# Optimization experiments

Hardware: AMD Instinct MI355X
Metric: run time of the kernel (lower is better)

Reference implementation:

```python
import jax, jax.numpy as jnp
import numpy as np

B, H, S, D = 4, 16, 2048, 64


def setup_inputs() -> dict:
    key = jax.random.key(0)
    kq, kk, kv = jax.random.split(key, 3)
    Q = jax.random.normal(kq, (B, H, S, D), dtype=jnp.float32)
    K = jax.random.normal(kk, (B, H, S, D), dtype=jnp.float32)
    V = jax.random.normal(kv, (B, H, S, D), dtype=jnp.float32)
    # causal mask, broadcasts over (B, H); True = keep, False (==0) = mask out
    mask = jnp.tril(jnp.ones((S, S), dtype=bool))
    return {"Q": Q, "K": K, "V": V, "mask": mask}


def reference(Q, K, V, mask):
    d_k = Q.shape[-1]
    scale = 1.0 / jnp.sqrt(jnp.asarray(d_k, dtype=Q.dtype))
    # [B,H,Sq,Sk] score matrix (the module materializes this fully)
    scores = jnp.einsum('bhqd,bhkd->bhqk', Q, K) * scale
    if mask is not None:
        scores = jnp.where(mask, scores, -jnp.inf)
    attn = jax.nn.softmax(scores, axis=-1)
    return jnp.einsum('bhqk,bhkd->bhqd', attn, V)
```

## Files before the change

### kernel.cpp

```cpp
#include <hip/hip_runtime.h>
#include <math.h>

namespace {

constexpr int SEQ   = 2048;
constexpr int DH    = 64;
constexpr int KVBLK = 64;
constexpr int BH    = 64;
constexpr size_t WS_NEED = (size_t)BH * SEQ * DH * 2  * 2 ;

typedef __bf16 bf16x8 __attribute__((ext_vector_type(8)));
typedef float  f32x16 __attribute__((ext_vector_type(16)));

union FragB { bf16x8 v; unsigned u[4]; };

__device__ __forceinline__ unsigned pack2(float a, float b) {
  unsigned r;
  asm("v_cvt_pk_bf16_f32 %0, %1, %2" : "=v"(r) : "v"(a), "v"(b));
  return r;
}

__device__ __forceinline__ unsigned short bf16c(float f) {
  union { float f; unsigned u; } v; v.f = f;
  unsigned r = v.u + 0x7fffu + ((v.u >> 16) & 1u);
  return (unsigned short)(r >> 16);
}

__device__ __forceinline__ void swap32(int a, int b, int &x, int &y) {
#if __has_builtin(__builtin_amdgcn_permlane32_swap)
  auto r = __builtin_amdgcn_permlane32_swap(a, b, false, false);
  x = r[0]; y = r[1];
#else
  const bool hi = ((threadIdx.x & 63) >= 32);
  const int sa = __shfl_xor(a, 32), sb = __shfl_xor(b, 32);
  x = hi ? sb : a;
  y = hi ? b  : sa;
#endif
}

__device__ __forceinline__ float xhalf_sum(float v) {
  int x, y; swap32(__float_as_int(v), __float_as_int(v), x, y);
  return __int_as_float(x) + __int_as_float(y);
}

__device__ __forceinline__ void gload16(const void* g, void* l) {
  __builtin_amdgcn_global_load_lds(
      (const __attribute__((address_space(1))) void*)g,
      (__attribute__((address_space(3))) void*)l, 16, 0, 0);
}

__global__ __launch_bounds__(256)
void prep(const float* __restrict__ Kg, const float* __restrict__ Vg,
          unsigned short* __restrict__ wsK, unsigned short* __restrict__ wsV)
{
  const int blk = blockIdx.x;
  const int bh  = blk & 63;
  const int t   = blk >> 6;
  const int tid = threadIdx.x;

  const float* Kb = Kg + (size_t)bh * SEQ * DH;
  unsigned short* wK = wsK + (size_t)bh * SEQ * DH;
#pragma unroll
  for (int i = 0; i < 2; ++i) {
    const int kc  = tid + i * 256;
    const int row = kc >> 3, c = kc & 7;
    const int csrc = c ^ (row & 7);
    const float* s = Kb + (size_t)(t*64 + row) * DH + csrc * 8;
    float4 a = *(const float4*)s, b2 = *(const float4*)(s + 4);
    uint4 w;
    w.x = pack2(a.x, a.y);   w.y = pack2(a.z, a.w);
    w.z = pack2(b2.x, b2.y); w.w = pack2(b2.z, b2.w);
    *(uint4*)&wK[(size_t)(t*64 + row) * DH + c * 8] = w;
  }

  __shared__ unsigned short vt[64 * 64];
  const float* Vb = Vg + (size_t)bh * SEQ * DH;
  {
    const int kv = tid >> 2;
    const int d0 = (tid & 3) * 16;
    const float* s = Vb + (size_t)(t*64 + kv) * DH + d0;
#pragma unroll
    for (int e = 0; e < 16; ++e) {
      const int d = d0 + e;
      const int slot = (kv >> 3) ^ (d & 7);
      vt[d*64 + slot*8 + (kv & 7)] = bf16c(s[e]);
    }
  }
  __syncthreads();
  unsigned short* wV = wsV + (size_t)bh * SEQ * DH + (size_t)t * 4096;
#pragma unroll
  for (int i = 0; i < 2; ++i) {
    const int o = (tid + i * 256) * 8;
    *(uint4*)&wV[o] = *(const uint4*)&vt[o];
  }
}

__global__ __launch_bounds__(256, 2)
void attn_fwd(const float* __restrict__ Qg, const unsigned short* __restrict__ wsK,
              const unsigned short* __restrict__ wsV, float* __restrict__ Og)
{
  const int b   = blockIdx.x;
  const int bh  = b & 63;
  const int qi  = 31 - (b >> 6);
  const int NT  = qi + 1;

  const int tid  = threadIdx.x;
  const int wv   = tid >> 6;
  const int rw   = wv & 1;
  const int kh   = wv >> 1;
  const int lane = tid & 63;
  const int l31  = lane & 31;
  const int hi   = lane >> 5;
  const int qloc = rw * 32 + l31;

  const float* Qp = Qg + (size_t)bh * SEQ * DH;
  const unsigned short* Kw = wsK + (size_t)bh * SEQ * DH;
  const unsigned short* Vw = wsV + (size_t)bh * SEQ * DH;
  float* Op = Og + (size_t)bh * SEQ * DH;

  __shared__ __align__(16) unsigned char smem[32768];

  const float qscale = 0.125f * 1.44269504088896f;
  FragB bq[4];
  {
    const float* src = Qp + (size_t)(qi*64 + rw*32 + l31) * DH + hi*8;
#pragma unroll
    for (int ks = 0; ks < 4; ++ks) {
      float4 f0 = *(const float4*)(src + ks*16);
      float4 f1 = *(const float4*)(src + ks*16 + 4);
      bq[ks].u[0] = pack2(f0.x*qscale, f0.y*qscale);
      bq[ks].u[1] = pack2(f0.z*qscale, f0.w*qscale);
      bq[ks].u[2] = pack2(f1.x*qscale, f1.y*qscale);
      bq[ks].u[3] = pack2(f1.z*qscale, f1.w*qscale);
    }
  }

  f32x16 oacc[2];
#pragma unroll
  for (int dt = 0; dt < 2; ++dt)
#pragma unroll
    for (int r = 0; r < 16; ++r) oacc[dt][r] = 0.f;
  float lpart = 0.f;

  auto stage = [&](int tile, int bufoff) {
    const unsigned short* gK = Kw + (size_t)tile * 4096 + wv*512 + lane*8;
    const unsigned short* gV = Vw + (size_t)tile * 4096 + wv*512 + lane*8;
    char* lb = (char*)smem + bufoff + wv*1024;
    gload16(gK,        lb);
    gload16(gK + 2048, lb + 4096);
    gload16(gV,        lb + 8192);
    gload16(gV + 2048, lb + 12288);
  };

  auto compute = [&](bool diag, int bufoff) {
    const unsigned short* Kl = (const unsigned short*)(smem + bufoff);
    const unsigned short* Vl = (const unsigned short*)(smem + bufoff + 8192);
    const int krow = kh*32 + l31;

    f32x16 st;
#pragma unroll
    for (int r = 0; r < 16; ++r) st[r] = 0.f;
    __builtin_amdgcn_s_setprio(1);
#pragma unroll
    for (int ks = 0; ks < 4; ++ks) {
      bf16x8 ak = *(const bf16x8*)&Kl[krow*64 + (((2*ks + hi) ^ (krow & 7)) * 8)];
      st = __builtin_amdgcn_mfma_f32_32x32x16_bf16(ak, bq[ks].v, st, 0, 0, 0);
    }
    __builtin_amdgcn_s_setprio(0);

    float p[16];
#pragma unroll
    for (int r = 0; r < 16; ++r) {
      float s = st[r];
      if (diag) {
        const int kvl = kh*32 + (r & 3) + 4*hi + 8*(r >> 2);
        if (kvl > qloc) s = -INFINITY;
      }
      const float e = exp2f(s);
      p[r] = e;
      lpart += e;
    }

    unsigned pk[8];
#pragma unroll
    for (int j2 = 0; j2 < 8; ++j2) pk[j2] = pack2(p[2*j2], p[2*j2 + 1]);

    FragB pa[2];
#pragma unroll
    for (int ks2 = 0; ks2 < 2; ++ks2) {
      const int gA = 2*ks2, gB = 2*ks2 + 1;
      int x0, y0, x1, y1;
      swap32((int)pk[2*gA],     (int)pk[2*gB],     x0, y0);
      swap32((int)pk[2*gA + 1], (int)pk[2*gB + 1], x1, y1);
      pa[ks2].u[0] = (unsigned)x0;
      pa[ks2].u[1] = (unsigned)x1;
      pa[ks2].u[2] = (unsigned)y0;
      pa[ks2].u[3] = (unsigned)y1;
    }

    __builtin_amdgcn_s_setprio(1);
#pragma unroll
    for (int dt = 0; dt < 2; ++dt) {
      const int d = dt*32 + l31;
#pragma unroll
      for (int ks2 = 0; ks2 < 2; ++ks2) {
        bf16x8 av = *(const bf16x8*)&Vl[d*64 + (((4*kh + 2*ks2 + hi) ^ (d & 7)) * 8)];
        oacc[dt] = __builtin_amdgcn_mfma_f32_32x32x16_bf16(av, pa[ks2].v, oacc[dt], 0, 0, 0);
      }
    }
    __builtin_amdgcn_s_setprio(0);
  };

  stage(0, 0);
  __syncthreads();

  for (int t = 0; t < NT; t += 2) {
    if (t + 1 < NT) stage(t + 1, 16384);
    compute(t == NT - 1, 0);
    __syncthreads();
    if (t + 1 < NT) {
      if (t + 2 < NT) stage(t + 2, 0);
      compute(t + 1 == NT - 1, 16384);
      __syncthreads();
    }
  }

  {
    float* reg0 = reinterpret_cast<float*>(smem);
    float* reg1 = reinterpret_cast<float*>(smem + 16384);
    float* myreg = rw ? reg1 : reg0;
    const int rb = l31 * 68;

    if (kh == 1) {
#pragma unroll
      for (int dt = 0; dt < 2; ++dt)
#pragma unroll
        for (int g4 = 0; g4 < 4; ++g4) {
          float4 w;
          w.x = oacc[dt][4*g4 + 0]; w.y = oacc[dt][4*g4 + 1];
          w.z = oacc[dt][4*g4 + 2]; w.w = oacc[dt][4*g4 + 3];
          *(float4*)&myreg[rb + dt*32 + 8*g4 + 4*hi] = w;
        }
      const float s1 = xhalf_sum(lpart);
      if (hi == 0) myreg[rb + 64] = s1;
    }
    __syncthreads();
    if (kh == 0) {
      const float linv = 1.0f / (xhalf_sum(lpart) + myreg[rb + 64]);
#pragma unroll
      for (int dt = 0; dt < 2; ++dt)
#pragma unroll
        for (int g4 = 0; g4 < 4; ++g4) {
          float4 v = *(const float4*)&myreg[rb + dt*32 + 8*g4 + 4*hi];
          v.x = (v.x + oacc[dt][4*g4 + 0]) * linv;
          v.y = (v.y + oacc[dt][4*g4 + 1]) * linv;
          v.z = (v.z + oacc[dt][4*g4 + 2]) * linv;
          v.w = (v.w + oacc[dt][4*g4 + 3]) * linv;
          *(float4*)&myreg[rb + dt*32 + 8*g4 + 4*hi] = v;
        }
    }
    __syncthreads();
    {
      float* dst = Op + (size_t)(qi * 64) * DH;
#pragma unroll
      for (int i = 0; i < 4; ++i) {
        const int f   = tid + i*256;
        const int row = f >> 4;
        const int ch  = f & 15;
        const float* srcrow = (row < 32) ? (reg0 + row*68) : (reg1 + (row-32)*68);
        float4 v = *(const float4*)&srcrow[ch*4];
        *(float4*)&dst[(size_t)row*DH + ch*4] = v;
      }
    }
  }
}

constexpr int PADB = 72;

__global__ __launch_bounds__(256, 2)
void attn_fb(const float* __restrict__ Qg, const float* __restrict__ Kg,
             const float* __restrict__ Vg, float* __restrict__ Og)
{
  const int b   = blockIdx.x;
  const int bh  = b & 63;
  const int qi  = 31 - (b >> 6);
  const int NT  = qi + 1;
  const int tid  = threadIdx.x;
  const int wv   = tid >> 6;
  const int rw   = wv & 1;
  const int kh   = wv >> 1;
  const int lane = tid & 63;
  const int l31  = lane & 31;
  const int hi   = lane >> 5;
  const int qloc = rw * 32 + l31;

  const size_t base = (size_t)bh * SEQ * DH;
  const float* Qp = Qg + base;
  const float* Kp = Kg + base;
  const float* Vp = Vg + base;
  float*       Op = Og + base;

  __shared__ __align__(16) unsigned char smem[18432];
  auto K_lds  = reinterpret_cast<__bf16(*)[PADB]>(smem);
  auto Vt_lds = reinterpret_cast<__bf16(*)[PADB]>(smem + 9216);

  const float qscale = 0.125f * 1.44269504088896f;
  FragB bq[4];
  {
    const float* src = Qp + (size_t)(qi*64 + rw*32 + l31) * DH + hi*8;
#pragma unroll
    for (int ks = 0; ks < 4; ++ks) {
      float4 f0 = *(const float4*)(src + ks*16);
      float4 f1 = *(const float4*)(src + ks*16 + 4);
      bq[ks].u[0] = pack2(f0.x*qscale, f0.y*qscale);
      bq[ks].u[1] = pack2(f0.z*qscale, f0.w*qscale);
      bq[ks].u[2] = pack2(f1.x*qscale, f1.y*qscale);
      bq[ks].u[3] = pack2(f1.z*qscale, f1.w*qscale);
    }
  }

  float4 kr[2][2];
  float  vr[16];
  const int kc8 = tid & 7;
  const int vd  = tid & 63;
  const int vk0 = (tid >> 6) * 16;

  auto load_tile = [&](int tile) {
    const int kvb = tile * KVBLK;
#pragma unroll
    for (int p = 0; p < 2; ++p) {
      const float* s = Kp + (size_t)(kvb + 32*p + (tid >> 3)) * DH + kc8*8;
      kr[p][0] = *(const float4*)s;
      kr[p][1] = *(const float4*)(s + 4);
    }
#pragma unroll
    for (int r = 0; r < 16; ++r)
      vr[r] = Vp[(size_t)(kvb + vk0 + r) * DH + vd];
  };

  auto store_tile = [&]() {
#pragma unroll
    for (int p = 0; p < 2; ++p) {
      uint4 w;
      w.x = pack2(kr[p][0].x, kr[p][0].y); w.y = pack2(kr[p][0].z, kr[p][0].w);
      w.z = pack2(kr[p][1].x, kr[p][1].y); w.w = pack2(kr[p][1].z, kr[p][1].w);
      *reinterpret_cast<uint4*>(&K_lds[32*p + (tid >> 3)][kc8*8]) = w;
    }
    uint4 w0, w1;
    w0.x = pack2(vr[0],  vr[1]);  w0.y = pack2(vr[2],  vr[3]);
    w0.z = pack2(vr[4],  vr[5]);  w0.w = pack2(vr[6],  vr[7]);
    w1.x = pack2(vr[8],  vr[9]);  w1.y = pack2(vr[10], vr[11]);
    w1.z = pack2(vr[12], vr[13]); w1.w = pack2(vr[14], vr[15]);
    *reinterpret_cast<uint4*>(&Vt_lds[vd][vk0])     = w0;
    *reinterpret_cast<uint4*>(&Vt_lds[vd][vk0 + 8]) = w1;
  };

  f32x16 oacc[2];
#pragma unroll
  for (int dt = 0; dt < 2; ++dt)
#pragma unroll
    for (int r = 0; r < 16; ++r) oacc[dt][r] = 0.f;
  float lpart = 0.f;

  load_tile(0);
  store_tile();
  __syncthreads();

  for (int t = 0; t < NT; ++t) {
    if (t + 1 < NT) load_tile(t + 1);
    const bool diag = (t == NT - 1);

    f32x16 st;
#pragma unroll
    for (int r = 0; r < 16; ++r) st[r] = 0.f;
#pragma unroll
    for (int ks = 0; ks < 4; ++ks) {
      bf16x8 ak = *(const bf16x8*)&K_lds[kh*32 + l31][ks*16 + hi*8];
      st = __builtin_amdgcn_mfma_f32_32x32x16_bf16(ak, bq[ks].v, st, 0, 0, 0);
    }

    float p[16];
#pragma unroll
    for (int r = 0; r < 16; ++r) {
      float s = st[r];
      if (diag) {
        const int kvl = kh*32 + (r & 3) + 4*hi + 8*(r >> 2);
        if (kvl > qloc) s = -INFINITY;
      }
      const float e = exp2f(s);
      p[r] = e;
      lpart += e;
    }

    unsigned pk[8];
#pragma unroll
    for (int j2 = 0; j2 < 8; ++j2) pk[j2] = pack2(p[2*j2], p[2*j2 + 1]);

    FragB pa[2];
#pragma unroll
    for (int ks2 = 0; ks2 < 2; ++ks2) {
      const int gA = 2*ks2, gB = 2*ks2 + 1;
      int x0, y0, x1, y1;
      swap32((int)pk[2*gA],     (int)pk[2*gB],     x0, y0);
      swap32((int)pk[2*gA + 1], (int)pk[2*gB + 1], x1, y1);
      pa[ks2].u[0] = (unsigned)x0;
      pa[ks2].u[1] = (unsigned)x1;
      pa[ks2].u[2] = (unsigned)y0;
      pa[ks2].u[3] = (unsigned)y1;
    }

#pragma unroll
    for (int dt = 0; dt < 2; ++dt)
#pragma unroll
      for (int ks2 = 0; ks2 < 2; ++ks2) {
        bf16x8 av = *(const bf16x8*)&Vt_lds[dt*32 + l31][kh*32 + ks2*16 + hi*8];
        oacc[dt] = __builtin_amdgcn_mfma_f32_32x32x16_bf16(av, pa[ks2].v, oacc[dt], 0, 0, 0);
      }

    __syncthreads();
    if (t + 1 < NT) {
      store_tile();
      __syncthreads();
    }
  }

  {
    float* reg0 = reinterpret_cast<float*>(smem);
    float* reg1 = reinterpret_cast<float*>(smem + 9216);
    float* myreg = rw ? reg1 : reg0;
    const int rb = l31 * 68;

    if (kh == 1) {
#pragma unroll
      for (int dt = 0; dt < 2; ++dt)
#pragma unroll
        for (int g4 = 0; g4 < 4; ++g4) {
          float4 w;
          w.x = oacc[dt][4*g4 + 0]; w.y = oacc[dt][4*g4 + 1];
          w.z = oacc[dt][4*g4 + 2]; w.w = oacc[dt][4*g4 + 3];
          *(float4*)&myreg[rb + dt*32 + 8*g4 + 4*hi] = w;
        }
      const float s1 = xhalf_sum(lpart);
      if (hi == 0) myreg[rb + 64] = s1;
    }
    __syncthreads();
    if (kh == 0) {
      const float linv = 1.0f / (xhalf_sum(lpart) + myreg[rb + 64]);
#pragma unroll
      for (int dt = 0; dt < 2; ++dt)
#pragma unroll
        for (int g4 = 0; g4 < 4; ++g4) {
          float4 v = *(const float4*)&myreg[rb + dt*32 + 8*g4 + 4*hi];
          v.x = (v.x + oacc[dt][4*g4 + 0]) * linv;
          v.y = (v.y + oacc[dt][4*g4 + 1]) * linv;
          v.z = (v.z + oacc[dt][4*g4 + 2]) * linv;
          v.w = (v.w + oacc[dt][4*g4 + 3]) * linv;
          *(float4*)&myreg[rb + dt*32 + 8*g4 + 4*hi] = v;
        }
    }
    __syncthreads();
    {
      float* dst = Op + (size_t)(qi * 64) * DH;
#pragma unroll
      for (int i = 0; i < 4; ++i) {
        const int f   = tid + i*256;
        const int row = f >> 4;
        const int ch  = f & 15;
        const float* srcrow = (row < 32) ? (reg0 + row*68) : (reg1 + (row-32)*68);
        float4 v = *(const float4*)&srcrow[ch*4];
        *(float4*)&dst[(size_t)row*DH + ch*4] = v;
      }
    }
  }
}

}

extern "C" void kernel_launch(void* const* d_in, const int* in_sizes, int n_in,
                              void* d_out, int out_size, void* d_ws, size_t ws_size,
                              hipStream_t stream) {
  const float* Q = (const float*)d_in[0];
  const float* K = (const float*)d_in[1];
  const float* V = (const float*)d_in[2];
  float* O = (float*)d_out;
  if (ws_size >= WS_NEED) {
    unsigned short* wsK = (unsigned short*)d_ws;
    unsigned short* wsV = wsK + (size_t)BH * SEQ * DH;
    prep<<<dim3(BH * 32), dim3(256), 0, stream>>>(K, V, wsK, wsV);
    attn_fwd<<<dim3(32 * BH), dim3(256), 0, stream>>>(Q, wsK, wsV, O);
  } else {
    attn_fb<<<dim3(32 * BH), dim3(256), 0, stream>>>(Q, K, V, O);
  }
}
```

Before: 81.23 us.

## Switch K/V staging to triple-buffered LDS pipeline with partial vmcnt waits

Replaces the double-buffered K/V staging loop with a three-slot LDS ring. Loads run two tiles ahead, and each step waits only until the current tile's loads have landed (vmcnt(4)), using a single barrier per iteration instead of a full __syncthreads after every compute. It also splits the row-sum accumulator into two partial sums to shorten the dependency chain. The cost is raising LDS to 48KB, which may reduce blocks per CU, and relying on manual vmcnt counting that assumes each stage issues exactly four loads.

```diff
diff --git a/kernel.cpp b/kernel.cpp
--- a/kernel.cpp
+++ b/kernel.cpp
@@ -118,7 +118,7 @@
   const unsigned short* Vw = wsV + (size_t)bh * SEQ * DH;
   float* Op = Og + (size_t)bh * SEQ * DH;
 
-  __shared__ __align__(16) unsigned char smem[32768];
+  __shared__ __align__(16) unsigned char smem[49152];
 
   const float qscale = 0.125f * 1.44269504088896f;
   FragB bq[4];
@@ -140,22 +140,24 @@
   for (int dt = 0; dt < 2; ++dt)
 #pragma unroll
     for (int r = 0; r < 16; ++r) oacc[dt][r] = 0.f;
-  float lpart = 0.f;
-
-  auto stage = [&](int tile, int bufoff) {
+  float lp0 = 0.f, lp1 = 0.f;
+
+  auto stage = [&](int tile) {
     const unsigned short* gK = Kw + (size_t)tile * 4096 + wv*512 + lane*8;
     const unsigned short* gV = Vw + (size_t)tile * 4096 + wv*512 + lane*8;
-    char* lb = (char*)smem + bufoff + wv*1024;
-    gload16(gK,        lb);
-    gload16(gK + 2048, lb + 4096);
-    gload16(gV,        lb + 8192);
-    gload16(gV + 2048, lb + 12288);
+    char* lK = (char*)smem + (tile % 3) * 8192 + wv*1024;
+    char* lV = (char*)smem + 24576 + (tile % 3) * 8192 + wv*1024;
+    gload16(gK,        lK);
+    gload16(gK + 2048, lK + 4096);
+    gload16(gV,        lV);
+    gload16(gV + 2048, lV + 4096);
   };
 
-  auto compute = [&](bool diag, int bufoff) {
-    const unsigned short* Kl = (const unsigned short*)(smem + bufoff);
-    const unsigned short* Vl = (const unsigned short*)(smem + bufoff + 8192);
-    const int krow = kh*32 + l31;
+  const int krow = kh*32 + l31;
+
+  auto compute = [&](bool diag, int buf) {
+    const unsigned short* Kl = (const unsigned short*)(smem + buf * 8192);
+    const unsigned short* Vl = (const unsigned short*)(smem + 24576 + buf * 8192);
 
     f32x16 st;
 #pragma unroll
@@ -178,7 +180,7 @@
       }
       const float e = exp2f(s);
       p[r] = e;
-      lpart += e;
+      if (r & 1) lp1 += e; else lp0 += e;
     }
 
     unsigned pk[8];
@@ -211,21 +213,23 @@
     __builtin_amdgcn_s_setprio(0);
   };
 
-  stage(0, 0);
+  stage(0);
+  if (NT > 1) stage(1);
+
+  for (int t = 0; t < NT; ++t) {
+    if (t + 1 < NT) {
+      asm volatile("s_waitcnt vmcnt(4)" ::: "memory");
+    } else {
+      asm volatile("s_waitcnt vmcnt(0)" ::: "memory");
+    }
+    __builtin_amdgcn_s_barrier();
+    if (t + 2 < NT) stage(t + 2);
+    compute(t == NT - 1, t % 3);
+  }
   __syncthreads();
 
-  for (int t = 0; t < NT; t += 2) {
-    if (t + 1 < NT) stage(t + 1, 16384);
-    compute(t == NT - 1, 0);
-    __syncthreads();
-    if (t + 1 < NT) {
-      if (t + 2 < NT) stage(t + 2, 0);
-      compute(t + 1 == NT - 1, 16384);
-      __syncthreads();
-    }
-  }
-
   {
+    const float lpart = lp0 + lp1;
     float* reg0 = reinterpret_cast<float*>(smem);
     float* reg1 = reinterpret_cast<float*>(smem + 16384);
     float* myreg = rw ? reg1 : reg0;
```

New measurement: 83.20 us. 1.02x slower.
